# Performance work log

Hardware: AMD Instinct MI355X
Metric: run time of the kernel (lower is better)

## Reference

```python
import jax, jax.numpy as jnp
import numpy as np

EPS = 1e-5

def _layernorm(x, g, b):
    mu = jnp.mean(x, axis=-1, keepdims=True)
    var = jnp.mean(jnp.square(x - mu), axis=-1, keepdims=True)
    return (x - mu) * jax.lax.rsqrt(var + EPS) * g + b

def setup_inputs() -> dict:
    key = jax.random.key(0)
    B, N, C, MID = 1, 512, 128, 128
    ks = jax.random.split(key, 12)
    s_c = 1.0 / np.sqrt(C)
    s_m = 1.0 / np.sqrt(MID)
    return {
        "act": jax.random.normal(ks[0], (B, N, N, C), dtype=jnp.float32),
        "mask": jnp.ones((B, N, N), dtype=jnp.float32),
        # input LayerNorm
        "ln_in_g": jnp.ones((C,), jnp.float32),
        "ln_in_b": jnp.zeros((C,), jnp.float32),
        # left/right projections and gates (Linear: y = x @ W + b)
        "wl": jax.random.normal(ks[1], (C, MID), jnp.float32) * s_c,
        "bl": jnp.zeros((MID,), jnp.float32),
        "wr": jax.random.normal(ks[2], (C, MID), jnp.float32) * s_c,
        "br": jnp.zeros((MID,), jnp.float32),
        "wgl": jax.random.normal(ks[3], (C, MID), jnp.float32) * s_c,
        "bgl": jnp.zeros((MID,), jnp.float32),
        "wgr": jax.random.normal(ks[4], (C, MID), jnp.float32) * s_c,
        "bgr": jnp.zeros((MID,), jnp.float32),
        # output gating linear (C -> C)
        "wgate": jax.random.normal(ks[5], (C, C), jnp.float32) * s_c,
        "bgate": jnp.zeros((C,), jnp.float32),
        # center LayerNorm (over MID)
        "ln_c_g": jnp.ones((MID,), jnp.float32),
        "ln_c_b": jnp.zeros((MID,), jnp.float32),
        # output projection (MID -> C)
        "wout": jax.random.normal(ks[6], (MID, C), jnp.float32) * s_m,
        "bout": jnp.zeros((C,), jnp.float32),
    }

def reference(act, mask, ln_in_g, ln_in_b, wl, bl, wr, br, wgl, bgl, wgr, bgr,
              wgate, bgate, ln_c_g, ln_c_b, wout, bout):
    x = _layernorm(act, ln_in_g, ln_in_b)          # [B,N,N,C]
    m = mask[..., None]                             # [B,N,N,1]
    left_proj = m * (x @ wl + bl) * jax.nn.sigmoid(x @ wgl + bgl)   # [B,N,N,MID]
    right_proj = m * (x @ wr + br) * jax.nn.sigmoid(x @ wgr + bgr)  # [B,N,N,MID]
    gate_values = x @ wgate + bgate                 # [B,N,N,C]
    # triangle outgoing: contract over k (second index of both)
    out = jnp.einsum('bikc,bjkc->bijc', left_proj, right_proj)      # [B,N,N,MID]
    out = _layernorm(out, ln_c_g, ln_c_b)
    out = out @ wout + bout                         # [B,N,N,C]
    return out * jax.nn.sigmoid(gate_values)
```

## Files before the change

kernel.cpp:

```cpp
#include <hip/hip_runtime.h>

#define NPOS 512
#define NN_ (512 * 512)

typedef unsigned short u16;
typedef __attribute__((ext_vector_type(8))) short bf16x8_t;
typedef __attribute__((ext_vector_type(4))) float f32x4_t;

__device__ __forceinline__ float bf2f(u16 u) {
  union { unsigned int i; float f; } v;
  v.i = ((unsigned int)u) << 16;
  return v.f;
}
__device__ __forceinline__ u16 f2bf(float f) {
  __bf16 h = (__bf16)f;
  return __builtin_bit_cast(unsigned short, h);
}
__device__ __forceinline__ float sigm(float x) { return 1.0f / (1.0f + __expf(-x)); }

__device__ __forceinline__ void gld_lds16(u16* lds, const u16* g) {
  __builtin_amdgcn_global_load_lds(
      (const __attribute__((address_space(1))) unsigned int*)g,
      (__attribute__((address_space(3))) unsigned int*)lds, 16, 0, 0);
}

__global__ __launch_bounds__(256) void k0_wt(const float* __restrict__ wl,
                                             const float* __restrict__ wgl,
                                             const float* __restrict__ wr,
                                             const float* __restrict__ wgr,
                                             const float* __restrict__ wgate,
                                             u16* __restrict__ wtbase) {
  int b = blockIdx.x;
  int wi = b >> 3;
  int o0 = (b & 7) * 16;
  const float* W = wi == 0 ? wl : wi == 1 ? wgl : wi == 2 ? wr : wi == 3 ? wgr : wgate;
  u16* dst = wtbase + wi * 16384;
  int t = threadIdx.x;
  int o = o0 + (t >> 4);
  int k0 = (t & 15) * 8;
  float v[8];
#pragma unroll
  for (int i = 0; i < 8; ++i) v[i] = W[(k0 + i) * 128 + o];
  ushort4 a, b4;
  a.x = f2bf(v[0]); a.y = f2bf(v[1]); a.z = f2bf(v[2]); a.w = f2bf(v[3]);
  b4.x = f2bf(v[4]); b4.y = f2bf(v[5]); b4.z = f2bf(v[6]); b4.w = f2bf(v[7]);
  *(ushort4*)(dst + o * 128 + k0) = a;
  *(ushort4*)(dst + o * 128 + k0 + 4) = b4;
}

__global__ __launch_bounds__(256) void k0b(const float* __restrict__ wout,
                                           u16* __restrict__ Wt6) {
  int o = blockIdx.x * 16 + (threadIdx.x >> 4);
  int k0 = (threadIdx.x & 15) * 8;
  float v[8];
#pragma unroll
  for (int i = 0; i < 8; ++i) v[i] = wout[(k0 + i) * 128 + o];
  ushort4 a, b4;
  a.x = f2bf(v[0]); a.y = f2bf(v[1]); a.z = f2bf(v[2]); a.w = f2bf(v[3]);
  b4.x = f2bf(v[4]); b4.y = f2bf(v[5]); b4.z = f2bf(v[6]); b4.w = f2bf(v[7]);
  *(ushort4*)(Wt6 + o * 128 + k0) = a;
  *(ushort4*)(Wt6 + o * 128 + k0 + 4) = b4;
}

__global__ __launch_bounds__(512, 4) void k2_fused(
    const float* __restrict__ act, const float* __restrict__ mask,
    const u16* __restrict__ wtbase,
    const float* __restrict__ ln_g, const float* __restrict__ ln_b,
    const float* __restrict__ bl, const float* __restrict__ bgl,
    const float* __restrict__ br, const float* __restrict__ bgr,
    u16* __restrict__ Lt, u16* __restrict__ Rt, u16* __restrict__ Gx) {
  __shared__ __align__(16) unsigned char smem[81920];
  u16* xn  = (u16*)smem;
  u16* wh0 = (u16*)(smem + 32768);
  u16* wh1 = (u16*)(smem + 49152);
  u16* ob  = (u16*)(smem + 65536);

  int tid = threadIdx.x;
  int l = tid & 63, w = tid >> 6;
  int wr_ = w >> 1, wc = w & 1;
  int lr = l & 15, lk = l >> 4;
  size_t p0 = (size_t)blockIdx.x * 128;

#define STAGE(i_, buf_)                                                     \
  {                                                                         \
    const u16* src = wtbase + ((i_) >> 1) * 16384 + ((i_) & 1) * 8192;      \
    _Pragma("unroll") for (int q = 0; q < 2; ++q) {                         \
      int s = q * 512 + tid;                                                \
      int row = s >> 4, j = (s & 15) ^ (row & 7);                           \
      gld_lds16((buf_) + s * 8, src + row * 128 + j * 8);                   \
    }                                                                       \
  }
#define ZERO(ACC)                                                           \
  { ACC[0][0] = (f32x4_t){0.f, 0.f, 0.f, 0.f};                              \
    ACC[0][1] = (f32x4_t){0.f, 0.f, 0.f, 0.f};                              \
    ACC[1][0] = (f32x4_t){0.f, 0.f, 0.f, 0.f};                              \
    ACC[1][1] = (f32x4_t){0.f, 0.f, 0.f, 0.f}; }
#define MFK(buf_, ACC, KT, AF0, AF1)                                        \
  {                                                                         \
    int kb = (KT) * 4 + lk;                                                 \
    int o0_ = wc * 32 + lr, o1_ = wc * 32 + 16 + lr;                        \
    bf16x8_t bfr0 = *(const bf16x8_t*)((buf_) + o0_ * 128 + ((kb ^ (o0_ & 7)) * 8)); \
    bf16x8_t bfr1 = *(const bf16x8_t*)((buf_) + o1_ * 128 + ((kb ^ (o1_ & 7)) * 8)); \
    ACC[0][0] = __builtin_amdgcn_mfma_f32_16x16x32_bf16(AF0, bfr0, ACC[0][0], 0, 0, 0); \
    ACC[0][1] = __builtin_amdgcn_mfma_f32_16x16x32_bf16(AF0, bfr1, ACC[0][1], 0, 0, 0); \
    ACC[1][0] = __builtin_amdgcn_mfma_f32_16x16x32_bf16(AF1, bfr0, ACC[1][0], 0, 0, 0); \
    ACC[1][1] = __builtin_amdgcn_mfma_f32_16x16x32_bf16(AF1, bfr1, ACC[1][1], 0, 0, 0); \
  }
#define MF(buf_, ACC)                                                       \
  MFK(buf_, ACC, 0, af00, af10)                                             \
  MFK(buf_, ACC, 1, af01, af11)                                             \
  MFK(buf_, ACC, 2, af02, af12)                                             \
  MFK(buf_, ACC, 3, af03, af13)
#define MFPAIR(ACCP, ACCG)                                                  \
  __builtin_amdgcn_s_setprio(1);                                            \
  ZERO(ACCP); MF(wh0, ACCP);                                                \
  ZERO(ACCG); MF(wh1, ACCG);                                                \
  __builtin_amdgcn_s_setprio(0);
#define EPW(ACCP, ACCG, Bp_, Bg_, obase_)                                   \
  {                                                                         \
    float bpv[2], bgv[2];                                                   \
    _Pragma("unroll") for (int n = 0; n < 2; ++n) {                         \
      int og = (obase_) + wc * 32 + n * 16 + lr;                            \
      bpv[n] = Bp_[og]; bgv[n] = Bg_[og];                                   \
    }                                                                       \
    _Pragma("unroll") for (int m = 0; m < 2; ++m) {                         \
      int p4 = wr_ * 32 + m * 16 + lk * 4;                                  \
      float4 mk = *(const float4*)(mask + p0 + p4);                         \
      int slot = p4 >> 3, off = p4 & 7;                                     \
      _Pragma("unroll") for (int n = 0; n < 2; ++n) {                       \
        int ol = wc * 32 + n * 16 + lr;                                     \
        ushort4 v;                                                          \
        v.x = f2bf(mk.x * (ACCP[m][n][0] + bpv[n]) * sigm(ACCG[m][n][0] + bgv[n])); \
        v.y = f2bf(mk.y * (ACCP[m][n][1] + bpv[n]) * sigm(ACCG[m][n][1] + bgv[n])); \
        v.z = f2bf(mk.z * (ACCP[m][n][2] + bpv[n]) * sigm(ACCG[m][n][2] + bgv[n])); \
        v.w = f2bf(mk.w * (ACCP[m][n][3] + bpv[n]) * sigm(ACCG[m][n][3] + bgv[n])); \
        *(ushort4*)(ob + ol * 128 + ((slot ^ (ol & 7)) << 3) + off) = v;    \
      }                                                                     \
    }                                                                       \
  }
#define EPS(Tdst_, obase_)                                                  \
  {                                                                         \
    _Pragma("unroll") for (int it = 0; it < 2; ++it) {                      \
      int s = it * 512 + tid;                                               \
      int ol = s >> 4, c8 = s & 15;                                         \
      *(uint4*)(Tdst_ + (size_t)((obase_) + ol) * NN_ + p0 + c8 * 8) =      \
          *(const uint4*)(ob + ol * 128 + ((c8 ^ (ol & 7)) << 3));          \
    }                                                                       \
  }

  STAGE(0, wh0);
  STAGE(2, wh1);

#pragma unroll
  for (int r = 0; r < 8; ++r) {
    int f = r * 512 + tid;
    int pos = f >> 5, c4 = f & 31;
    float4 v = *(const float4*)(act + (p0 + pos) * 128 + c4 * 4);
    float s1 = v.x + v.y + v.z + v.w;
    float s2 = v.x * v.x + v.y * v.y + v.z * v.z + v.w * v.w;
#pragma unroll
    for (int m = 1; m < 32; m <<= 1) {
      s1 += __shfl_xor(s1, m);
      s2 += __shfl_xor(s2, m);
    }
    float mu = s1 * (1.0f / 128.0f);
    float rstd = rsqrtf(s2 * (1.0f / 128.0f) - mu * mu + 1e-5f);
    int cb = c4 * 4;
    float4 gg = *(const float4*)(ln_g + cb);
    float4 bb = *(const float4*)(ln_b + cb);
    ushort4 o4;
    o4.x = f2bf((v.x - mu) * rstd * gg.x + bb.x);
    o4.y = f2bf((v.y - mu) * rstd * gg.y + bb.y);
    o4.z = f2bf((v.z - mu) * rstd * gg.z + bb.z);
    o4.w = f2bf((v.w - mu) * rstd * gg.w + bb.w);
    int c8 = c4 >> 1, off = (c4 & 1) * 4;
    *(ushort4*)(xn + pos * 128 + ((c8 ^ (pos & 7)) << 3) + off) = o4;
  }
  __syncthreads();

  bf16x8_t af00, af01, af02, af03, af10, af11, af12, af13;
  {
    int row0 = wr_ * 32 + lr;
    int row1 = wr_ * 32 + 16 + lr;
    const u16* x0 = xn + row0 * 128;
    const u16* x1 = xn + row1 * 128;
    af00 = *(const bf16x8_t*)(x0 + (((0 * 4 + lk) ^ (row0 & 7)) * 8));
    af01 = *(const bf16x8_t*)(x0 + (((1 * 4 + lk) ^ (row0 & 7)) * 8));
    af02 = *(const bf16x8_t*)(x0 + (((2 * 4 + lk) ^ (row0 & 7)) * 8));
    af03 = *(const bf16x8_t*)(x0 + (((3 * 4 + lk) ^ (row0 & 7)) * 8));
    af10 = *(const bf16x8_t*)(x1 + (((0 * 4 + lk) ^ (row1 & 7)) * 8));
    af11 = *(const bf16x8_t*)(x1 + (((1 * 4 + lk) ^ (row1 & 7)) * 8));
    af12 = *(const bf16x8_t*)(x1 + (((2 * 4 + lk) ^ (row1 & 7)) * 8));
    af13 = *(const bf16x8_t*)(x1 + (((3 * 4 + lk) ^ (row1 & 7)) * 8));
  }

#pragma unroll
  for (int q = 0; q < 4; ++q) {
    int s = q * 512 + tid;
    int row = s >> 4, c8 = s & 15;
    *(uint4*)(Gx + (p0 + row) * 128 + c8 * 8) =
        *(const uint4*)(xn + row * 128 + c8 * 8);
  }

  f32x4_t ap[2][2], ag[2][2];

  MFPAIR(ap, ag);
  __syncthreads();
  STAGE(1, wh0);
  STAGE(3, wh1);
  EPW(ap, ag, bl, bgl, 0);
  __syncthreads();
  EPS(Lt, 0);

  MFPAIR(ap, ag);
  __syncthreads();
  STAGE(4, wh0);
  STAGE(6, wh1);
  EPW(ap, ag, bl, bgl, 64);
  __syncthreads();
  EPS(Lt, 64);

  MFPAIR(ap, ag);
  __syncthreads();
  STAGE(5, wh0);
  STAGE(7, wh1);
  EPW(ap, ag, br, bgr, 0);
  __syncthreads();
  EPS(Rt, 0);

  MFPAIR(ap, ag);
  __syncthreads();
  EPW(ap, ag, br, bgr, 64);
  __syncthreads();
  EPS(Rt, 64);
#undef STAGE
#undef ZERO
#undef MFK
#undef MF
#undef MFPAIR
#undef EPW
#undef EPS
}

__global__ __launch_bounds__(256, 4) void k3_einsum_mfma(const u16* __restrict__ Lt,
                                                         const u16* __restrict__ Rt,
                                                         u16* __restrict__ Ot) {
  __shared__ __align__(16) u16 smem[2 * 128 * 64];
  u16* La = smem;
  u16* Rb = smem + 128 * 64;

  int tid = threadIdx.x;
  int bid = blockIdx.x;
  int swz = (bid & 7) * 256 + (bid >> 3);
  int c = swz >> 4;
  int t = swz & 15;
  int i0 = (t >> 2) << 7, j0 = (t & 3) << 7;
  const u16* Lg = Lt + (size_t)c * NN_ + (size_t)i0 * 512;
  const u16* Rg = Rt + (size_t)c * NN_ + (size_t)j0 * 512;

  int l = tid & 63, w = tid >> 6;
  int wr = w >> 1, wc = w & 1;
  int lr = l & 15, lk = l >> 4;

  f32x4_t acc[4][4];
#pragma unroll
  for (int m = 0; m < 4; ++m)
#pragma unroll
    for (int n = 0; n < 4; ++n) acc[m][n] = (f32x4_t){0.f, 0.f, 0.f, 0.f};

  for (int kt = 0; kt < 512; kt += 64) {
#pragma unroll
    for (int q = 0; q < 4; ++q) {
      int s = q * 256 + tid;
      int row = s >> 3;
      int k8 = (s & 7) ^ (row & 7);
      gld_lds16(La + s * 8, Lg + (size_t)row * 512 + kt + k8 * 8);
      gld_lds16(Rb + s * 8, Rg + (size_t)row * 512 + kt + k8 * 8);
    }
    __syncthreads();

    __builtin_amdgcn_s_setprio(1);
#pragma unroll
    for (int ks = 0; ks < 2; ++ks) {
      int kb = ks * 4 + lk;
      bf16x8_t af[4], bf[4];
#pragma unroll
      for (int m = 0; m < 4; ++m) {
        int row = wr * 64 + m * 16 + lr;
        af[m] = *(const bf16x8_t*)(La + row * 64 + ((kb ^ (row & 7)) * 8));
      }
#pragma unroll
      for (int n = 0; n < 4; ++n) {
        int row = wc * 64 + n * 16 + lr;
        bf[n] = *(const bf16x8_t*)(Rb + row * 64 + ((kb ^ (row & 7)) * 8));
      }
#pragma unroll
      for (int m = 0; m < 4; ++m)
#pragma unroll
        for (int n = 0; n < 4; ++n)
          acc[m][n] = __builtin_amdgcn_mfma_f32_16x16x32_bf16(af[m], bf[n], acc[m][n], 0, 0, 0);
    }
    __builtin_amdgcn_s_setprio(0);
    __syncthreads();
  }

  u16* ob = smem;
#pragma unroll
  for (int m = 0; m < 4; ++m) {
    int row0 = wr * 64 + m * 16 + lk * 4;
#pragma unroll
    for (int n = 0; n < 4; ++n) {
      int col = (wc * 64 + n * 16 + lr) ^ (lk << 4);
#pragma unroll
      for (int r = 0; r < 4; ++r)
        ob[(row0 + r) * 128 + col] = f2bf(acc[m][n][r]);
    }
  }
  __syncthreads();
#pragma unroll
  for (int it = 0; it < 8; ++it) {
    int s = it * 256 + tid;
    int row = s >> 4, c8 = s & 15;
    int g = (row >> 2) & 3;
    const u16* src = ob + row * 128 + ((c8 * 8) ^ (g << 4));
    *(uint4*)(Ot + (size_t)c * NN_ + (size_t)(i0 + row) * 512 + j0 + c8 * 8) =
        *(const uint4*)src;
  }
}

__global__ __launch_bounds__(512, 4) void k4_mfma(const u16* __restrict__ Ot,
                                                  const u16* __restrict__ Gx,
                                                  const u16* __restrict__ wtbase,
                                                  const u16* __restrict__ Wt6,
                                                  const float* __restrict__ bgate,
                                                  const float* __restrict__ gc,
                                                  const float* __restrict__ bc,
                                                  const float* __restrict__ bout,
                                                  float* __restrict__ out) {
  __shared__ __align__(16) unsigned char smem[70656];
  u16* xg = (u16*)smem;
  u16* wg = (u16*)(smem + 32768);
  u16* ot = (u16*)smem;
  u16* ws = (u16*)(smem + 32768);
  float* ps = (float*)(smem + 65536);
  float* pss = (float*)(smem + 67584);
  float2* munr = (float2*)(smem + 69632);

  int tid = threadIdx.x;
  int l = tid & 63, w = tid >> 6;
  int wr = w >> 1, wc = w & 1;
  int lr = l & 15, lk = l >> 4;
  size_t p0 = (size_t)blockIdx.x * 128;
  int i_row = (int)(p0 >> 9);
  int j0 = (int)(p0 & 511);

#pragma unroll
  for (int q = 0; q < 4; ++q) {
    int s = q * 512 + tid;
    int row = s >> 4, c8 = s & 15;
    gld_lds16(xg + s * 8, Gx + (p0 + row) * 128 + c8 * 8);
  }
  {
    const u16* wsrc = wtbase + 4 * 16384;
#pragma unroll
    for (int q = 0; q < 4; ++q) {
      int s = q * 512 + tid;
      int row = s >> 4, j = (s & 15) ^ (row & 7);
      gld_lds16(wg + s * 8, wsrc + row * 128 + j * 8);
    }
  }
  __syncthreads();

  f32x4_t gacc[2][4];
#pragma unroll
  for (int m = 0; m < 2; ++m)
#pragma unroll
    for (int n = 0; n < 4; ++n) gacc[m][n] = (f32x4_t){0.f, 0.f, 0.f, 0.f};

  __builtin_amdgcn_s_setprio(1);
#pragma unroll
  for (int kt = 0; kt < 4; ++kt) {
    int kb = kt * 4 + lk;
    bf16x8_t af[2], bf[4];
#pragma unroll
    for (int m = 0; m < 2; ++m) {
      int row = wr * 32 + m * 16 + lr;
      af[m] = *(const bf16x8_t*)(xg + row * 128 + ((kb ^ (row & 7)) * 8));
    }
#pragma unroll
    for (int n = 0; n < 4; ++n) {
      int o = wc * 64 + n * 16 + lr;
      bf[n] = *(const bf16x8_t*)(wg + o * 128 + ((kb ^ (o & 7)) * 8));
    }
#pragma unroll
    for (int m = 0; m < 2; ++m)
#pragma unroll
      for (int n = 0; n < 4; ++n)
        gacc[m][n] = __builtin_amdgcn_mfma_f32_16x16x32_bf16(af[m], bf[n], gacc[m][n], 0, 0, 0);
  }
  __builtin_amdgcn_s_setprio(0);

  ushort4 gb[2][4];
#pragma unroll
  for (int n = 0; n < 4; ++n) {
    float bg = bgate[wc * 64 + n * 16 + lr];
#pragma unroll
    for (int m = 0; m < 2; ++m) {
      gb[m][n].x = f2bf(gacc[m][n][0] + bg);
      gb[m][n].y = f2bf(gacc[m][n][1] + bg);
      gb[m][n].z = f2bf(gacc[m][n][2] + bg);
      gb[m][n].w = f2bf(gacc[m][n][3] + bg);
    }
  }
  __syncthreads();

#pragma unroll
  for (int q = 0; q < 4; ++q) {
    int s = q * 512 + tid;
    int cc = s >> 4, j = s & 15;
    gld_lds16(ot + s * 8, Ot + (size_t)cc * NN_ + (size_t)i_row * 512 + j0 + j * 8);
  }
#pragma unroll
  for (int q = 0; q < 4; ++q) {
    int s = q * 512 + tid;
    int o = s >> 4, j = (s & 15) ^ (o & 7);
    gld_lds16(ws + s * 8, Wt6 + o * 128 + j * 8);
  }
  __syncthreads();

  int g = tid >> 7, pos = tid & 127;
  float vals[32];
  float s1 = 0.0f, s2 = 0.0f;
#pragma unroll
  for (int m = 0; m < 32; ++m) {
    float v = bf2f(ot[(g * 32 + m) * 128 + pos]);
    vals[m] = v;
    s1 += v;
    s2 += v * v;
  }
  ps[g * 128 + pos] = s1;
  pss[g * 128 + pos] = s2;
  __syncthreads();
  if (tid < 128) {
    float a = ps[tid] + ps[128 + tid] + ps[256 + tid] + ps[384 + tid];
    float b = pss[tid] + pss[128 + tid] + pss[256 + tid] + pss[384 + tid];
    float mu = a * (1.0f / 128.0f);
    float rstd = rsqrtf(b * (1.0f / 128.0f) - mu * mu + 1e-5f);
    munr[tid] = make_float2(mu, rstd);
  }
  __syncthreads();
  float2 mr = munr[pos];

  u16* xn = ot;
#pragma unroll
  for (int mm = 0; mm < 4; ++mm) {
    int c8 = g * 4 + mm;
    ushort4 va, vb;
    int cb = c8 * 8;
    va.x = f2bf((vals[mm * 8 + 0] - mr.x) * mr.y * gc[cb + 0] + bc[cb + 0]);
    va.y = f2bf((vals[mm * 8 + 1] - mr.x) * mr.y * gc[cb + 1] + bc[cb + 1]);
    va.z = f2bf((vals[mm * 8 + 2] - mr.x) * mr.y * gc[cb + 2] + bc[cb + 2]);
    va.w = f2bf((vals[mm * 8 + 3] - mr.x) * mr.y * gc[cb + 3] + bc[cb + 3]);
    vb.x = f2bf((vals[mm * 8 + 4] - mr.x) * mr.y * gc[cb + 4] + bc[cb + 4]);
    vb.y = f2bf((vals[mm * 8 + 5] - mr.x) * mr.y * gc[cb + 5] + bc[cb + 5]);
    vb.z = f2bf((vals[mm * 8 + 6] - mr.x) * mr.y * gc[cb + 6] + bc[cb + 6]);
    vb.w = f2bf((vals[mm * 8 + 7] - mr.x) * mr.y * gc[cb + 7] + bc[cb + 7]);
    int slot = (c8 ^ (pos & 7)) * 8;
    *(ushort4*)(xn + pos * 128 + slot) = va;
    *(ushort4*)(xn + pos * 128 + slot + 4) = vb;
  }
  __syncthreads();

  f32x4_t acc[2][4];
#pragma unroll
  for (int m = 0; m < 2; ++m)
#pragma unroll
    for (int n = 0; n < 4; ++n) acc[m][n] = (f32x4_t){0.f, 0.f, 0.f, 0.f};

  __builtin_amdgcn_s_setprio(1);
#pragma unroll
  for (int kt = 0; kt < 4; ++kt) {
    int kb = kt * 4 + lk;
    bf16x8_t af[2], bf[4];
#pragma unroll
    for (int m = 0; m < 2; ++m) {
      int row = wr * 32 + m * 16 + lr;
      af[m] = *(const bf16x8_t*)(xn + row * 128 + ((kb ^ (row & 7)) * 8));
    }
#pragma unroll
    for (int n = 0; n < 4; ++n) {
      int o = wc * 64 + n * 16 + lr;
      bf[n] = *(const bf16x8_t*)(ws + o * 128 + ((kb ^ (o & 7)) * 8));
    }
#pragma unroll
    for (int m = 0; m < 2; ++m)
#pragma unroll
      for (int n = 0; n < 4; ++n)
        acc[m][n] = __builtin_amdgcn_mfma_f32_16x16x32_bf16(af[m], bf[n], acc[m][n], 0, 0, 0);
  }
  __builtin_amdgcn_s_setprio(0);

  float* os = (float*)(smem + 32768);
#pragma unroll
  for (int h = 0; h < 2; ++h) {
    __syncthreads();
    if ((wr >> 1) == h) {
#pragma unroll
      for (int n = 0; n < 4; ++n) {
        int o = wc * 64 + n * 16 + lr;
        float bo = bout[o];
#pragma unroll
        for (int m = 0; m < 2; ++m) {
          int p = (wr & 1) * 32 + m * 16 + lk * 4;
          float gv[4] = {sigm(bf2f(gb[m][n].x)), sigm(bf2f(gb[m][n].y)),
                         sigm(bf2f(gb[m][n].z)), sigm(bf2f(gb[m][n].w))};
#pragma unroll
          for (int r = 0; r < 4; ++r) {
            int row = p + r;
            os[row * 128 + (o ^ (((row >> 2) & 7) << 4))] = (acc[m][n][r] + bo) * gv[r];
          }
        }
      }
    }
    __syncthreads();
#pragma unroll
    for (int it = 0; it < 4; ++it) {
      int s = it * 512 + tid;
      int row = s >> 5, sl = s & 31;
      float4 v = *(const float4*)(os + row * 128 + ((sl * 4) ^ (((row >> 2) & 7) << 4)));
      *(float4*)(out + (p0 + h * 64 + row) * 128 + sl * 4) = v;
    }
  }
}

extern "C" void kernel_launch(void* const* d_in, const int* in_sizes, int n_in,
                              void* d_out, int out_size, void* d_ws, size_t ws_size,
                              hipStream_t stream) {
  const float* act    = (const float*)d_in[0];
  const float* mask   = (const float*)d_in[1];
  const float* ln_in_g = (const float*)d_in[2];
  const float* ln_in_b = (const float*)d_in[3];
  const float* wl     = (const float*)d_in[4];
  const float* bl     = (const float*)d_in[5];
  const float* wr     = (const float*)d_in[6];
  const float* br     = (const float*)d_in[7];
  const float* wgl    = (const float*)d_in[8];
  const float* bgl    = (const float*)d_in[9];
  const float* wgr    = (const float*)d_in[10];
  const float* bgr    = (const float*)d_in[11];
  const float* wgate  = (const float*)d_in[12];
  const float* bgate  = (const float*)d_in[13];
  const float* ln_c_g = (const float*)d_in[14];
  const float* ln_c_b = (const float*)d_in[15];
  const float* wout   = (const float*)d_in[16];
  const float* bout   = (const float*)d_in[17];
  float* out = (float*)d_out;

  char* ws = (char*)d_ws;
  const size_t SEG = 1ull << 26;
  u16* Lt  = (u16*)(ws);
  u16* Rt  = (u16*)(ws + 1 * SEG);
  u16* Gx  = (u16*)(ws + 2 * SEG);
  u16* Ot  = (u16*)(ws + 3 * SEG);
  u16* Wt6 = Lt;

  u16* wtbase = (u16*)((char*)d_out + (size_t)out_size * 4 - 5 * 32768);

  k0_wt<<<dim3(40), dim3(256), 0, stream>>>(wl, wgl, wr, wgr, wgate, wtbase);
  k2_fused<<<dim3(2048), dim3(512), 0, stream>>>(act, mask, wtbase, ln_in_g, ln_in_b,
                                                 bl, bgl, br, bgr, Lt, Rt, Gx);
  k3_einsum_mfma<<<dim3(2048), dim3(256), 0, stream>>>(Lt, Rt, Ot);
  k0b<<<dim3(8), dim3(256), 0, stream>>>(wout, Wt6);
  k4_mfma<<<dim3(2048), dim3(512), 0, stream>>>(Ot, Gx, wtbase, Wt6, bgate,
                                                ln_c_g, ln_c_b, bout, out);
}
```

Measured before the change: 248.9 us.

## Process two 128-position tiles per k2 block to reuse staged weights

Each k2_fused block now handles 256 positions as two 128-row tiles, and the grid is halved. Each staged weight slice is used for both tiles before the next slice is staged, so weight staging traffic per position is halved. The second tile reads its A fragments straight from LDS instead of holding them in registers. Gx is now written directly during the LayerNorm pass instead of in a separate copy loop. In exchange there are more barriers per block and fewer blocks to spread across the CUs.

Result: faster. 242.7 us, median of 2 (-2.5%).

```diff
diff --git a/kernel.cpp b/kernel.cpp
--- a/kernel.cpp
+++ b/kernel.cpp
@@ -79,7 +79,8 @@
   int l = tid & 63, w = tid >> 6;
   int wr_ = w >> 1, wc = w & 1;
   int lr = l & 15, lk = l >> 4;
-  size_t p0 = (size_t)blockIdx.x * 128;
+  size_t p0 = (size_t)blockIdx.x * 256;
+  size_t p1 = p0 + 128;
 
 #define STAGE(i_, buf_)                                                     \
   {                                                                         \
@@ -95,7 +96,7 @@
     ACC[0][1] = (f32x4_t){0.f, 0.f, 0.f, 0.f};                              \
     ACC[1][0] = (f32x4_t){0.f, 0.f, 0.f, 0.f};                              \
     ACC[1][1] = (f32x4_t){0.f, 0.f, 0.f, 0.f}; }
-#define MFK(buf_, ACC, KT, AF0, AF1)                                        \
+#define MFK0(buf_, ACC, KT, AF0, AF1)                                       \
   {                                                                         \
     int kb = (KT) * 4 + lk;                                                 \
     int o0_ = wc * 32 + lr, o1_ = wc * 32 + 16 + lr;                        \
@@ -106,17 +107,28 @@
     ACC[1][0] = __builtin_amdgcn_mfma_f32_16x16x32_bf16(AF1, bfr0, ACC[1][0], 0, 0, 0); \
     ACC[1][1] = __builtin_amdgcn_mfma_f32_16x16x32_bf16(AF1, bfr1, ACC[1][1], 0, 0, 0); \
   }
-#define MF(buf_, ACC)                                                       \
-  MFK(buf_, ACC, 0, af00, af10)                                             \
-  MFK(buf_, ACC, 1, af01, af11)                                             \
-  MFK(buf_, ACC, 2, af02, af12)                                             \
-  MFK(buf_, ACC, 3, af03, af13)
-#define MFPAIR(ACCP, ACCG)                                                  \
-  __builtin_amdgcn_s_setprio(1);                                            \
-  ZERO(ACCP); MF(wh0, ACCP);                                                \
-  ZERO(ACCG); MF(wh1, ACCG);                                                \
-  __builtin_amdgcn_s_setprio(0);
-#define EPW(ACCP, ACCG, Bp_, Bg_, obase_)                                   \
+#define MF0(buf_, ACC)                                                      \
+  MFK0(buf_, ACC, 0, af00, af10)                                            \
+  MFK0(buf_, ACC, 1, af01, af11)                                            \
+  MFK0(buf_, ACC, 2, af02, af12)                                            \
+  MFK0(buf_, ACC, 3, af03, af13)
+#define MFK1(buf_, ACC, KT)                                                 \
+  {                                                                         \
+    int kb = (KT) * 4 + lk;                                                 \
+    int r0_ = wr_ * 32 + lr, r1_ = wr_ * 32 + 16 + lr;                      \
+    bf16x8_t a0_ = *(const bf16x8_t*)(xn + r0_ * 128 + ((kb ^ (r0_ & 7)) * 8)); \
+    bf16x8_t a1_ = *(const bf16x8_t*)(xn + r1_ * 128 + ((kb ^ (r1_ & 7)) * 8)); \
+    int o0_ = wc * 32 + lr, o1_ = wc * 32 + 16 + lr;                        \
+    bf16x8_t bfr0 = *(const bf16x8_t*)((buf_) + o0_ * 128 + ((kb ^ (o0_ & 7)) * 8)); \
+    bf16x8_t bfr1 = *(const bf16x8_t*)((buf_) + o1_ * 128 + ((kb ^ (o1_ & 7)) * 8)); \
+    ACC[0][0] = __builtin_amdgcn_mfma_f32_16x16x32_bf16(a0_, bfr0, ACC[0][0], 0, 0, 0); \
+    ACC[0][1] = __builtin_amdgcn_mfma_f32_16x16x32_bf16(a0_, bfr1, ACC[0][1], 0, 0, 0); \
+    ACC[1][0] = __builtin_amdgcn_mfma_f32_16x16x32_bf16(a1_, bfr0, ACC[1][0], 0, 0, 0); \
+    ACC[1][1] = __builtin_amdgcn_mfma_f32_16x16x32_bf16(a1_, bfr1, ACC[1][1], 0, 0, 0); \
+  }
+#define MF1(buf_, ACC)                                                      \
+  MFK1(buf_, ACC, 0) MFK1(buf_, ACC, 1) MFK1(buf_, ACC, 2) MFK1(buf_, ACC, 3)
+#define EPW(ACCP, ACCG, Bp_, Bg_, obase_, TB_)                              \
   {                                                                         \
     float bpv[2], bgv[2];                                                   \
     _Pragma("unroll") for (int n = 0; n < 2; ++n) {                         \
@@ -125,7 +137,7 @@
     }                                                                       \
     _Pragma("unroll") for (int m = 0; m < 2; ++m) {                         \
       int p4 = wr_ * 32 + m * 16 + lk * 4;                                  \
-      float4 mk = *(const float4*)(mask + p0 + p4);                         \
+      float4 mk = *(const float4*)(mask + (TB_) + p4);                      \
       int slot = p4 >> 3, off = p4 & 7;                                     \
       _Pragma("unroll") for (int n = 0; n < 2; ++n) {                       \
         int ol = wc * 32 + n * 16 + lr;                                     \
@@ -138,44 +150,65 @@
       }                                                                     \
     }                                                                       \
   }
-#define EPS(Tdst_, obase_)                                                  \
+#define EPS(Tdst_, obase_, TB_)                                             \
   {                                                                         \
     _Pragma("unroll") for (int it = 0; it < 2; ++it) {                      \
       int s = it * 512 + tid;                                               \
       int ol = s >> 4, c8 = s & 15;                                         \
-      *(uint4*)(Tdst_ + (size_t)((obase_) + ol) * NN_ + p0 + c8 * 8) =      \
+      *(uint4*)(Tdst_ + (size_t)((obase_) + ol) * NN_ + (TB_) + c8 * 8) =   \
           *(const uint4*)(ob + ol * 128 + ((c8 ^ (ol & 7)) << 3));          \
     }                                                                       \
   }
+#define LN_TILE(TB_)                                                        \
+  _Pragma("unroll")                                                         \
+  for (int r = 0; r < 8; ++r) {                                             \
+    int f = r * 512 + tid;                                                  \
+    int pos = f >> 5, c4 = f & 31;                                          \
+    float4 v = *(const float4*)(act + ((TB_) + pos) * 128 + c4 * 4);        \
+    float s1 = v.x + v.y + v.z + v.w;                                       \
+    float s2 = v.x * v.x + v.y * v.y + v.z * v.z + v.w * v.w;               \
+    _Pragma("unroll") for (int m = 1; m < 32; m <<= 1) {                    \
+      s1 += __shfl_xor(s1, m);                                              \
+      s2 += __shfl_xor(s2, m);                                              \
+    }                                                                       \
+    float mu = s1 * (1.0f / 128.0f);                                        \
+    float rstd = rsqrtf(s2 * (1.0f / 128.0f) - mu * mu + 1e-5f);            \
+    int cb = c4 * 4;                                                        \
+    float4 gg = *(const float4*)(ln_g + cb);                                \
+    float4 bb = *(const float4*)(ln_b + cb);                                \
+    ushort4 o4;                                                             \
+    o4.x = f2bf((v.x - mu) * rstd * gg.x + bb.x);                           \
+    o4.y = f2bf((v.y - mu) * rstd * gg.y + bb.y);                           \
+    o4.z = f2bf((v.z - mu) * rstd * gg.z + bb.z);                           \
+    o4.w = f2bf((v.w - mu) * rstd * gg.w + bb.w);                           \
+    int c8 = c4 >> 1, off = (c4 & 1) * 4;                                   \
+    int so = pos * 128 + ((c8 ^ (pos & 7)) << 3) + off;                     \
+    *(ushort4*)(xn + so) = o4;                                              \
+    *(ushort4*)(Gx + (size_t)(TB_) * 128 + so) = o4;                        \
+  }
+#define SECTION(Bp_, Bg_, obase_, Tdst_, DO_STAGE_, s0_, s1_)               \
+  __builtin_amdgcn_s_setprio(1);                                            \
+  ZERO(ap); MF0(wh0, ap);                                                   \
+  ZERO(ag); MF0(wh1, ag);                                                   \
+  __builtin_amdgcn_s_setprio(0);                                            \
+  __syncthreads();                                                          \
+  EPW(ap, ag, Bp_, Bg_, obase_, p0);                                        \
+  __syncthreads();                                                          \
+  EPS(Tdst_, obase_, p0);                                                   \
+  __builtin_amdgcn_s_setprio(1);                                            \
+  ZERO(ap); MF1(wh0, ap);                                                   \
+  ZERO(ag); MF1(wh1, ag);                                                   \
+  __builtin_amdgcn_s_setprio(0);                                            \
+  __syncthreads();                                                          \
+  if (DO_STAGE_) { STAGE(s0_, wh0); STAGE(s1_, wh1); }                      \
+  EPW(ap, ag, Bp_, Bg_, obase_, p1);                                        \
+  __syncthreads();                                                          \
+  EPS(Tdst_, obase_, p1);
 
   STAGE(0, wh0);
   STAGE(2, wh1);
 
-#pragma unroll
-  for (int r = 0; r < 8; ++r) {
-    int f = r * 512 + tid;
-    int pos = f >> 5, c4 = f & 31;
-    float4 v = *(const float4*)(act + (p0 + pos) * 128 + c4 * 4);
-    float s1 = v.x + v.y + v.z + v.w;
-    float s2 = v.x * v.x + v.y * v.y + v.z * v.z + v.w * v.w;
-#pragma unroll
-    for (int m = 1; m < 32; m <<= 1) {
-      s1 += __shfl_xor(s1, m);
-      s2 += __shfl_xor(s2, m);
-    }
-    float mu = s1 * (1.0f / 128.0f);
-    float rstd = rsqrtf(s2 * (1.0f / 128.0f) - mu * mu + 1e-5f);
-    int cb = c4 * 4;
-    float4 gg = *(const float4*)(ln_g + cb);
-    float4 bb = *(const float4*)(ln_b + cb);
-    ushort4 o4;
-    o4.x = f2bf((v.x - mu) * rstd * gg.x + bb.x);
-    o4.y = f2bf((v.y - mu) * rstd * gg.y + bb.y);
-    o4.z = f2bf((v.z - mu) * rstd * gg.z + bb.z);
-    o4.w = f2bf((v.w - mu) * rstd * gg.w + bb.w);
-    int c8 = c4 >> 1, off = (c4 & 1) * 4;
-    *(ushort4*)(xn + pos * 128 + ((c8 ^ (pos & 7)) << 3) + off) = o4;
-  }
+  LN_TILE(p0);
   __syncthreads();
 
   bf16x8_t af00, af01, af02, af03, af10, af11, af12, af13;
@@ -193,53 +226,27 @@
     af12 = *(const bf16x8_t*)(x1 + (((2 * 4 + lk) ^ (row1 & 7)) * 8));
     af13 = *(const bf16x8_t*)(x1 + (((3 * 4 + lk) ^ (row1 & 7)) * 8));
   }
-
-#pragma unroll
-  for (int q = 0; q < 4; ++q) {
-    int s = q * 512 + tid;
-    int row = s >> 4, c8 = s & 15;
-    *(uint4*)(Gx + (p0 + row) * 128 + c8 * 8) =
-        *(const uint4*)(xn + row * 128 + c8 * 8);
-  }
+  __syncthreads();
+
+  LN_TILE(p1);
+  __syncthreads();
 
   f32x4_t ap[2][2], ag[2][2];
 
-  MFPAIR(ap, ag);
-  __syncthreads();
-  STAGE(1, wh0);
-  STAGE(3, wh1);
-  EPW(ap, ag, bl, bgl, 0);
-  __syncthreads();
-  EPS(Lt, 0);
-
-  MFPAIR(ap, ag);
-  __syncthreads();
-  STAGE(4, wh0);
-  STAGE(6, wh1);
-  EPW(ap, ag, bl, bgl, 64);
-  __syncthreads();
-  EPS(Lt, 64);
-
-  MFPAIR(ap, ag);
-  __syncthreads();
-  STAGE(5, wh0);
-  STAGE(7, wh1);
-  EPW(ap, ag, br, bgr, 0);
-  __syncthreads();
-  EPS(Rt, 0);
-
-  MFPAIR(ap, ag);
-  __syncthreads();
-  EPW(ap, ag, br, bgr, 64);
-  __syncthreads();
-  EPS(Rt, 64);
+  SECTION(bl, bgl, 0,  Lt, 1, 1, 3);
+  SECTION(bl, bgl, 64, Lt, 1, 4, 6);
+  SECTION(br, bgr, 0,  Rt, 1, 5, 7);
+  SECTION(br, bgr, 64, Rt, 0, 0, 0);
 #undef STAGE
 #undef ZERO
-#undef MFK
-#undef MF
-#undef MFPAIR
+#undef MFK0
+#undef MF0
+#undef MFK1
+#undef MF1
 #undef EPW
 #undef EPS
+#undef LN_TILE
+#undef SECTION
 }
 
 __global__ __launch_bounds__(256, 4) void k3_einsum_mfma(const u16* __restrict__ Lt,
@@ -567,7 +574,7 @@
   u16* wtbase = (u16*)((char*)d_out + (size_t)out_size * 4 - 5 * 32768);
 
   k0_wt<<<dim3(40), dim3(256), 0, stream>>>(wl, wgl, wr, wgr, wgate, wtbase);
-  k2_fused<<<dim3(2048), dim3(512), 0, stream>>>(act, mask, wtbase, ln_in_g, ln_in_b,
+  k2_fused<<<dim3(1024), dim3(512), 0, stream>>>(act, mask, wtbase, ln_in_g, ln_in_b,
                                                  bl, bgl, br, bgr, Lt, Rt, Gx);
   k3_einsum_mfma<<<dim3(2048), dim3(256), 0, stream>>>(Lt, Rt, Ot);
   k0b<<<dim3(8), dim3(256), 0, stream>>>(wout, Wt6);
```
